# Optimization experiments

Hardware: AMD Instinct MI355X
Metric: run time of the kernel (lower is better)

## Reference

```python
import jax, jax.numpy as jnp
import numpy as np

N_NODES = 100000
N_EDGES = 300000
D = 256
N_LAYERS = 9
LN_EPS = 1e-5


def _mlp(h, w1, b1, w2, b2, ln_g, ln_b):
    # torch Linear: y = x @ W.T + b ; W is [out, in]
    h = jax.nn.relu(jnp.einsum('nd,hd->nh', h, w1) + b1)
    h = jnp.einsum('nh,oh->no', h, w2) + b2
    mu = jnp.mean(h, axis=-1, keepdims=True)
    var = jnp.mean(jnp.square(h - mu), axis=-1, keepdims=True)
    return (h - mu) * jax.lax.rsqrt(var + LN_EPS) * ln_g + ln_b


def setup_inputs() -> dict:
    key = jax.random.key(0)
    ks = jax.random.split(key, 16)
    s = 0.05  # small init scale for numerical sanity across 9 layers
    inp = {
        'x': jax.random.normal(ks[0], (N_NODES, D), dtype=jnp.float32),
        'edge_attr': jax.random.normal(ks[1], (N_EDGES, D), dtype=jnp.float32),
        'edge_fc1_w': jax.random.normal(ks[2], (N_LAYERS, D, D), dtype=jnp.float32) * s,
        'edge_fc1_b': jnp.zeros((N_LAYERS, D), dtype=jnp.float32),
        'edge_fc2_w': jax.random.normal(ks[3], (N_LAYERS, D, D), dtype=jnp.float32) * s,
        'edge_fc2_b': jnp.zeros((N_LAYERS, D), dtype=jnp.float32),
        'edge_ln_g': jnp.ones((N_LAYERS, D), dtype=jnp.float32),
        'edge_ln_b': jnp.zeros((N_LAYERS, D), dtype=jnp.float32),
        'node_fc1_w': jax.random.normal(ks[4], (N_LAYERS, D, D), dtype=jnp.float32) * s,
        'node_fc1_b': jnp.zeros((N_LAYERS, D), dtype=jnp.float32),
        'node_fc2_w': jax.random.normal(ks[5], (N_LAYERS, D, D), dtype=jnp.float32) * s,
        'node_fc2_b': jnp.zeros((N_LAYERS, D), dtype=jnp.float32),
        'node_ln_g': jnp.ones((N_LAYERS, D), dtype=jnp.float32),
        'node_ln_b': jnp.zeros((N_LAYERS, D), dtype=jnp.float32),
        'edge_index': jax.random.randint(ks[6], (2, N_EDGES), 0, N_NODES, dtype=jnp.int32),
    }
    return inp


def reference(x, edge_attr, edge_fc1_w, edge_fc1_b, edge_fc2_w, edge_fc2_b,
              edge_ln_g, edge_ln_b, node_fc1_w, node_fc1_b, node_fc2_w, node_fc2_b,
              node_ln_g, node_ln_b, edge_index):
    src = edge_index[0]  # x_j
    tgt = edge_index[1]  # aggregation target (aggr='add')
    for l in range(N_LAYERS):
        # edge MLP is applied to the ORIGINAL edge_attr in every layer
        e = _mlp(edge_attr, edge_fc1_w[l], edge_fc1_b[l], edge_fc2_w[l], edge_fc2_b[l],
                 edge_ln_g[l], edge_ln_b[l])
        msg = x[src] + e                               # [E, D] gather + add
        aggr = jax.ops.segment_sum(msg, tgt, num_segments=N_NODES)  # scatter-add
        upd = _mlp(aggr, node_fc1_w[l], node_fc1_b[l], node_fc2_w[l], node_fc2_b[l],
                   node_ln_g[l], node_ln_b[l])
        x = upd + x                                    # residual
    return x
```

## Files before the change

kernel.cpp:

```cpp
#include <hip/hip_runtime.h>
#include <stdint.h>

#define DD 256
#define NEDGE 300000
#define NNODE 100000
#define NLAY 9
#define LN_EPS 1e-5f

typedef __attribute__((ext_vector_type(8))) short bf16x8;
typedef __attribute__((ext_vector_type(4))) short s16x4;
typedef __attribute__((ext_vector_type(4))) float f32x4;
typedef __attribute__((ext_vector_type(4))) int i32x4;

static __device__ __forceinline__ short f2bf(float f) {
  union { float f; uint32_t u; } v; v.f = f;
  uint32_t r = (v.u + 0x7FFFu + ((v.u >> 16) & 1u)) >> 16;
  return (short)(uint16_t)r;
}
static __device__ __forceinline__ float bf2f(short s) {
  union { uint32_t u; float f; } v; v.u = ((uint32_t)(uint16_t)s) << 16;
  return v.f;
}
static __device__ __forceinline__ int addbf2(int a, int b) {
  const float a0 = bf2f((short)(a & 0xffff)), a1 = bf2f((short)(((uint32_t)a) >> 16));
  const float b0 = bf2f((short)(b & 0xffff)), b1 = bf2f((short)(((uint32_t)b) >> 16));
  const uint16_t r0 = (uint16_t)f2bf(a0 + b0), r1 = (uint16_t)f2bf(a1 + b1);
  return (int)(((uint32_t)r1 << 16) | r0);
}

static __device__ __forceinline__ void gld16(const void* g, void* l) {
  __builtin_amdgcn_global_load_lds((const __attribute__((address_space(1))) void*)g,
                                   (__attribute__((address_space(3))) void*)l, 16, 0, 0);
}

__global__ void cvtw_kernel(const float* __restrict__ src, short* __restrict__ dst, int nmat) {
  const int total = nmat * 8192;
  for (int j = blockIdx.x * blockDim.x + threadIdx.x; j < total; j += gridDim.x * blockDim.x) {
    const int m = j >> 13;
    const int jj = j & 8191;
    const int col = jj & 255;
    const int kq = jj >> 8;
    const float* s = src + (size_t)m * 65536 + col * 256 + kq * 8;
    const f32x4 u0 = *(const f32x4*)(s);
    const f32x4 u1 = *(const f32x4*)(s + 4);
    bf16x8 o;
#pragma unroll
    for (int q = 0; q < 4; ++q) { o[q] = f2bf(u0[q]); o[q + 4] = f2bf(u1[q]); }
    *(bf16x8*)(dst + (size_t)j * 8) = o;
  }
}

template<bool A_BF16, bool NODE>
__global__ __launch_bounds__(512, 4) void mlp_kernel(
    const void* __restrict__ Ain, const int* __restrict__ rowmap,
    const int* __restrict__ offs, const int* __restrict__ ssrc,
    const short* __restrict__ XbIn,
    const short* __restrict__ W1t, const short* __restrict__ W2t,
    const float* __restrict__ B1, const float* __restrict__ B2,
    const float* __restrict__ LG, const float* __restrict__ LB,
    short* __restrict__ OutB, float* __restrict__ OutF,
    short* __restrict__ XbOut, int M) {
  extern __shared__ char smem[];
  char* Abuf = smem + 32768;
  float* redbuf = (float*)(smem + 65536);
  const int tid = threadIdx.x;
  const int lane = tid & 63;
  const int wv = tid >> 6;
  const int wm = wv >> 2, wn = wv & 3;
  const int l15 = lane & 15, lq = lane >> 4;
  const int cbase = wn * 64;
  const int r0 = blockIdx.x * 64;

  auto stageW = [&](const short* Wt, int s, int slot) {
#pragma unroll
    for (int j = 0; j < 2; ++j) {
      const int c = tid + 512 * j;
      gld16(Wt + ((size_t)s * 1024 + c) * 8, smem + slot * 16384 + c * 16);
    }
  };

  stageW(W1t, 0, 0);

  if (NODE) {
    const short* efs = (const short*)Ain;
    const int r = tid & 63;
    const int j = tid >> 6;
    const int n = min(r0 + r, M - 1);
    const int beg = offs[n], end = offs[n + 1];
    float s[4][8];
#pragma unroll
    for (int c = 0; c < 4; ++c)
#pragma unroll
      for (int q = 0; q < 8; ++q) s[c][q] = 0.f;
    for (int p = beg; p < end; ++p) {
      const int src = ssrc[p];
#pragma unroll
      for (int c = 0; c < 4; ++c) {
        const int kq = j * 4 + c;
        const bf16x8 ev = *(const bf16x8*)(efs + (size_t)p * DD + kq * 8);
        const bf16x8 xv = *(const bf16x8*)(XbIn + (size_t)src * DD + kq * 8);
#pragma unroll
        for (int q = 0; q < 8; ++q) s[c][q] += bf2f(ev[q]) + bf2f(xv[q]);
      }
    }
#pragma unroll
    for (int c = 0; c < 4; ++c) {
      const int kq = j * 4 + c;
      bf16x8 o;
#pragma unroll
      for (int q = 0; q < 8; ++q) o[q] = f2bf(s[c][q]);
      *(bf16x8*)(Abuf + (kq * 64 + r) * 16) = o;
    }
  } else if (A_BF16) {
    const short* A = (const short*)Ain;
#pragma unroll
    for (int j = 0; j < 4; ++j) {
      const int c = tid + 512 * j;
      const int row = c & 63, kq = c >> 6;
      const int gr = min(r0 + row, M - 1);
      gld16(A + (size_t)gr * DD + kq * 8, Abuf + c * 16);
    }
  } else {
    const float* A = (const float*)Ain;
#pragma unroll
    for (int j = 0; j < 4; ++j) {
      const int c = tid + 512 * j;
      const int row = c & 63, kq = c >> 6;
      const int gr0 = min(r0 + row, M - 1);
      const int gr = rowmap ? rowmap[gr0] : gr0;
      const f32x4 u0 = *(const f32x4*)(A + (size_t)gr * DD + kq * 8);
      const f32x4 u1 = *(const f32x4*)(A + (size_t)gr * DD + kq * 8 + 4);
      bf16x8 o;
#pragma unroll
      for (int q = 0; q < 4; ++q) { o[q] = f2bf(u0[q]); o[q + 4] = f2bf(u1[q]); }
      *(bf16x8*)(Abuf + c * 16) = o;
    }
  }
  __syncthreads();

  f32x4 acc[2][4];
#pragma unroll
  for (int mi = 0; mi < 2; ++mi)
#pragma unroll
    for (int ni = 0; ni < 4; ++ni) acc[mi][ni] = (f32x4){0.f, 0.f, 0.f, 0.f};

#pragma unroll
  for (int s = 0; s < 8; ++s) {
    if (s < 7) stageW(W1t, s + 1, (s + 1) & 1);
    else       stageW(W2t, 0, 0);
    const char* wb = smem + (s & 1) * 16384;
    bf16x8 a[2], b[4];
#pragma unroll
    for (int mi = 0; mi < 2; ++mi)
      a[mi] = *(const bf16x8*)(Abuf + (((s * 4 + lq) * 64) + wm * 32 + mi * 16 + l15) * 16);
#pragma unroll
    for (int ni = 0; ni < 4; ++ni)
      b[ni] = *(const bf16x8*)(wb + lq * 4096 + (cbase + ni * 16 + l15) * 16);
#pragma unroll
    for (int ni = 0; ni < 4; ++ni)
#pragma unroll
      for (int mi = 0; mi < 2; ++mi)
        acc[mi][ni] = __builtin_amdgcn_mfma_f32_16x16x32_bf16(b[ni], a[mi], acc[mi][ni], 0, 0, 0);
    __syncthreads();
  }

  short* hid = (short*)Abuf;
  {
    f32x4 b1q[4];
#pragma unroll
    for (int ni = 0; ni < 4; ++ni)
      b1q[ni] = *(const f32x4*)(B1 + cbase + ni * 16 + lq * 4);
#pragma unroll
    for (int mi = 0; mi < 2; ++mi) {
      const int r = wm * 32 + mi * 16 + l15;
#pragma unroll
      for (int ni = 0; ni < 4; ++ni) {
        const int c4 = cbase + ni * 16 + lq * 4;
        s16x4 o;
#pragma unroll
        for (int i = 0; i < 4; ++i) {
          o[i] = f2bf(fmaxf(acc[mi][ni][i] + b1q[ni][i], 0.f));
          acc[mi][ni][i] = 0.f;
        }
        *(s16x4*)((char*)hid + r * 512 + (((c4 >> 3) ^ (r & 7)) << 4) + (c4 & 7) * 2) = o;
      }
    }
  }
  __syncthreads();

#pragma unroll
  for (int s = 0; s < 8; ++s) {
    if (s < 7) stageW(W2t, s + 1, (s + 1) & 1);
    const char* wb = smem + (s & 1) * 16384;
    bf16x8 a[2], b[4];
#pragma unroll
    for (int mi = 0; mi < 2; ++mi) {
      const int r = wm * 32 + mi * 16 + l15;
      a[mi] = *(const bf16x8*)((const char*)hid + r * 512 + ((((s * 4 + lq)) ^ (r & 7)) << 4));
    }
#pragma unroll
    for (int ni = 0; ni < 4; ++ni)
      b[ni] = *(const bf16x8*)(wb + lq * 4096 + (cbase + ni * 16 + l15) * 16);
#pragma unroll
    for (int ni = 0; ni < 4; ++ni)
#pragma unroll
      for (int mi = 0; mi < 2; ++mi)
        acc[mi][ni] = __builtin_amdgcn_mfma_f32_16x16x32_bf16(b[ni], a[mi], acc[mi][ni], 0, 0, 0);
    __syncthreads();
  }

  f32x4 b2q[4];
#pragma unroll
  for (int ni = 0; ni < 4; ++ni)
    b2q[ni] = *(const f32x4*)(B2 + cbase + ni * 16 + lq * 4);
  float mean_[2], inv_[2];
#pragma unroll
  for (int mi = 0; mi < 2; ++mi) {
    float s1 = 0.f, s2 = 0.f;
#pragma unroll
    for (int ni = 0; ni < 4; ++ni)
#pragma unroll
      for (int i = 0; i < 4; ++i) {
        const float v = acc[mi][ni][i] + b2q[ni][i];
        s1 += v; s2 += v * v;
      }
    s1 += __shfl_xor(s1, 16); s2 += __shfl_xor(s2, 16);
    s1 += __shfl_xor(s1, 32); s2 += __shfl_xor(s2, 32);
    mean_[mi] = s1; inv_[mi] = s2;
  }
  if (lq == 0) {
#pragma unroll
    for (int mi = 0; mi < 2; ++mi) {
      const int r = wm * 32 + mi * 16 + l15;
      redbuf[(r * 4 + wn) * 2 + 0] = mean_[mi];
      redbuf[(r * 4 + wn) * 2 + 1] = inv_[mi];
    }
  }
  __syncthreads();
#pragma unroll
  for (int mi = 0; mi < 2; ++mi) {
    const int r = wm * 32 + mi * 16 + l15;
    float t1 = 0.f, t2 = 0.f;
#pragma unroll
    for (int w = 0; w < 4; ++w) {
      t1 += redbuf[(r * 4 + w) * 2 + 0];
      t2 += redbuf[(r * 4 + w) * 2 + 1];
    }
    const float mean = t1 * (1.f / 256.f);
    const float var = t2 * (1.f / 256.f) - mean * mean;
    mean_[mi] = mean;
    inv_[mi] = rsqrtf(var + LN_EPS);
  }

  f32x4 gq[4], bq[4];
#pragma unroll
  for (int ni = 0; ni < 4; ++ni) {
    gq[ni] = *(const f32x4*)(LG + cbase + ni * 16 + lq * 4);
    bq[ni] = *(const f32x4*)(LB + cbase + ni * 16 + lq * 4);
  }

  if (NODE) {
    const bool wantF = (OutF != nullptr);
    if (!wantF) {
      short* ob = (short*)Abuf;
#pragma unroll
      for (int mi = 0; mi < 2; ++mi) {
        const int r = wm * 32 + mi * 16 + l15;
#pragma unroll
        for (int ni = 0; ni < 4; ++ni) {
          const int c4 = cbase + ni * 16 + lq * 4;
          s16x4 o;
#pragma unroll
          for (int i = 0; i < 4; ++i)
            o[i] = f2bf((acc[mi][ni][i] + b2q[ni][i] - mean_[mi]) * inv_[mi] * gq[ni][i] + bq[ni][i]);
          *(s16x4*)((char*)ob + r * 512 + (((c4 >> 3) ^ (r & 7)) << 4) + (c4 & 7) * 2) = o;
        }
      }
      __syncthreads();
#pragma unroll
      for (int j = 0; j < 4; ++j) {
        const int gg = tid + 512 * j;
        const int row = gg >> 5, Lg = gg & 31;
        const int grow = r0 + row;
        if (grow < M) {
          const i32x4 yv = *(const i32x4*)((const short*)ob + row * DD + ((Lg ^ (row & 7)) << 3));
          i32x4 xv = *(const i32x4*)(XbIn + (size_t)grow * DD + Lg * 8);
#pragma unroll
          for (int q = 0; q < 4; ++q) xv[q] = addbf2(yv[q], xv[q]);
          *(i32x4*)(XbOut + (size_t)grow * DD + Lg * 8) = xv;
        }
      }
    } else {
      float* ob = (float*)Abuf;
#pragma unroll
      for (int h = 0; h < 2; ++h) {
        if ((cbase >> 7) == h) {
#pragma unroll
          for (int mi = 0; mi < 2; ++mi) {
            const int r = wm * 32 + mi * 16 + l15;
#pragma unroll
            for (int ni = 0; ni < 4; ++ni) {
              const int cl4 = cbase - h * 128 + ni * 16 + lq * 4;
              f32x4 y;
#pragma unroll
              for (int i = 0; i < 4; ++i)
                y[i] = (acc[mi][ni][i] + b2q[ni][i] - mean_[mi]) * inv_[mi] * gq[ni][i] + bq[ni][i];
              *(f32x4*)((char*)ob + r * 512 + ((((cl4 >> 2) ^ (r & 7))) << 4)) = y;
            }
          }
        }
        __syncthreads();
#pragma unroll
        for (int j = 0; j < 4; ++j) {
          const int gg = tid + 512 * j;
          const int row = gg >> 5, Lc = gg & 31;
          const int grow = r0 + row;
          if (grow < M) {
            f32x4 v = *(const f32x4*)(ob + row * 128 + ((Lc ^ (row & 7)) << 2));
            const s16x4 xr = *(const s16x4*)(XbIn + (size_t)grow * DD + h * 128 + Lc * 4);
            v.x += bf2f(xr.x); v.y += bf2f(xr.y); v.z += bf2f(xr.z); v.w += bf2f(xr.w);
            *(f32x4*)(OutF + (size_t)grow * DD + h * 128 + Lc * 4) = v;
          }
        }
        if (h == 0) __syncthreads();
      }
    }
  } else {
    short* ob = (short*)Abuf;
#pragma unroll
    for (int mi = 0; mi < 2; ++mi) {
      const int r = wm * 32 + mi * 16 + l15;
#pragma unroll
      for (int ni = 0; ni < 4; ++ni) {
        const int c4 = cbase + ni * 16 + lq * 4;
        s16x4 o;
#pragma unroll
        for (int i = 0; i < 4; ++i)
          o[i] = f2bf((acc[mi][ni][i] + b2q[ni][i] - mean_[mi]) * inv_[mi] * gq[ni][i] + bq[ni][i]);
        *(s16x4*)((char*)ob + r * 512 + (((c4 >> 3) ^ (r & 7)) << 4) + (c4 & 7) * 2) = o;
      }
    }
    __syncthreads();
#pragma unroll
    for (int j = 0; j < 4; ++j) {
      const int gg = tid + 512 * j;
      const int row = gg >> 5, Lg = gg & 31;
      const int grow = r0 + row;
      if (grow < M) {
        const i32x4 v = *(const i32x4*)((const short*)ob + row * DD + ((Lg ^ (row & 7)) << 3));
        *(i32x4*)(OutB + (size_t)grow * DD + Lg * 8) = v;
      }
    }
  }
}

__global__ void count_kernel(const int* __restrict__ tgt, int* __restrict__ deg) {
  const int e = blockIdx.x * 256 + threadIdx.x;
  if (e < NEDGE) atomicAdd(&deg[tgt[e]], 1);
}

__global__ __launch_bounds__(256) void scan1_kernel(
    const int* __restrict__ deg, int* __restrict__ locex, int* __restrict__ bsum) {
  __shared__ int sh[256];
  const int t = threadIdx.x, b = blockIdx.x;
  const int idx = b * 256 + t;
  const int v = (idx < NNODE) ? deg[idx] : 0;
  sh[t] = v;
  __syncthreads();
#pragma unroll
  for (int off = 1; off < 256; off <<= 1) {
    const int add = (t >= off) ? sh[t - off] : 0;
    __syncthreads();
    sh[t] += add;
    __syncthreads();
  }
  if (idx < NNODE) locex[idx] = sh[t] - v;
  if (t == 255) bsum[b] = sh[255];
}

__global__ __launch_bounds__(512) void scan2_kernel(int* __restrict__ bsum, int nb) {
  __shared__ int sh[512];
  const int t = threadIdx.x;
  const int v = (t < nb) ? bsum[t] : 0;
  sh[t] = v;
  __syncthreads();
#pragma unroll
  for (int off = 1; off < 512; off <<= 1) {
    const int add = (t >= off) ? sh[t - off] : 0;
    __syncthreads();
    sh[t] += add;
    __syncthreads();
  }
  if (t < nb) bsum[t] = sh[t] - v;
}

__global__ __launch_bounds__(256) void scan3_kernel(
    const int* __restrict__ locex, const int* __restrict__ bsum,
    int* __restrict__ offs, int* __restrict__ cur) {
  const int idx = blockIdx.x * 256 + threadIdx.x;
  if (idx < NNODE) {
    const int o = locex[idx] + bsum[blockIdx.x];
    offs[idx] = o;
    cur[idx] = o;
  }
  if (idx == 0) offs[NNODE] = NEDGE;
}

__global__ void fill_kernel(const int* __restrict__ src, const int* __restrict__ tgt,
                            int* cur, int* seid, int* ssrc) {
  const int e = blockIdx.x * 256 + threadIdx.x;
  if (e < NEDGE) {
    const int t = tgt[e];
    const int p = atomicAdd(&cur[t], 1);
    seid[p] = e;
    ssrc[p] = src[e];
  }
}

__global__ void cvt4_kernel(const float* __restrict__ src, short* __restrict__ dst, int n4) {
  for (int i = blockIdx.x * blockDim.x + threadIdx.x; i < n4; i += gridDim.x * blockDim.x) {
    const f32x4 v = ((const f32x4*)src)[i];
    s16x4 o;
    o.x = f2bf(v.x); o.y = f2bf(v.y); o.z = f2bf(v.z); o.w = f2bf(v.w);
    ((s16x4*)dst)[i] = o;
  }
}

__global__ __launch_bounds__(256) void gather_cvt_kernel(
    const float* __restrict__ src, const int* __restrict__ perm,
    short* __restrict__ dst, int n) {
  const int w = (blockIdx.x * blockDim.x + threadIdx.x) >> 6;
  if (w >= n) return;
  const int lane = threadIdx.x & 63;
  const f32x4 v = *(const f32x4*)(src + (size_t)perm[w] * DD + lane * 4);
  s16x4 o; o.x = f2bf(v.x); o.y = f2bf(v.y); o.z = f2bf(v.z); o.w = f2bf(v.w);
  *(s16x4*)(dst + (size_t)w * DD + lane * 4) = o;
}

extern "C" void kernel_launch(void* const* d_in, const int* in_sizes, int n_in,
                              void* d_out, int out_size, void* d_ws, size_t ws_size,
                              hipStream_t stream) {
  const float* x_in = (const float*)d_in[0];
  const float* ea_f = (const float*)d_in[1];
  const float* e1w = (const float*)d_in[2];
  const float* e1b = (const float*)d_in[3];
  const float* e2w = (const float*)d_in[4];
  const float* e2b = (const float*)d_in[5];
  const float* elg = (const float*)d_in[6];
  const float* elb = (const float*)d_in[7];
  const float* n1w = (const float*)d_in[8];
  const float* n1b = (const float*)d_in[9];
  const float* n2w = (const float*)d_in[10];
  const float* n2b = (const float*)d_in[11];
  const float* nlg = (const float*)d_in[12];
  const float* nlb = (const float*)d_in[13];
  const int* eidx = (const int*)d_in[14];
  float* x = (float*)d_out;

  char* p = (char*)d_ws;
  auto take = [&](size_t bytes) {
    char* r = p;
    p += (bytes + 255) & ~(size_t)255;
    return r;
  };
  short* efeat = (short*)take((size_t)NEDGE * DD * 2);
  short* xbA = (short*)take((size_t)NNODE * DD * 2);
  short* xbB = (short*)take((size_t)NNODE * DD * 2);
  short* we1t = (short*)take((size_t)NLAY * DD * DD * 2);
  short* we2t = (short*)take((size_t)NLAY * DD * DD * 2);
  short* wn1t = (short*)take((size_t)NLAY * DD * DD * 2);
  short* wn2t = (short*)take((size_t)NLAY * DD * DD * 2);
  int* deg = (int*)take((size_t)NNODE * 4);
  int* offs = (int*)take((size_t)(NNODE + 1) * 4);
  int* cur = (int*)take((size_t)NNODE * 4);
  int* seid = (int*)take((size_t)NEDGE * 4);
  int* ssrc = (int*)take((size_t)NEDGE * 4);
  int* locex = (int*)take((size_t)(NNODE + 256) * 4);
  int* bsum = (int*)take(512 * 4);
  short* eab = (short*)take((size_t)NEDGE * DD * 2);
  const bool use_eab = ((size_t)(p - (char*)d_ws) <= ws_size);

  const int SMEM = 67584;
  hipFuncSetAttribute((const void*)mlp_kernel<true, false>,
                      hipFuncAttributeMaxDynamicSharedMemorySize, SMEM);
  hipFuncSetAttribute((const void*)mlp_kernel<false, false>,
                      hipFuncAttributeMaxDynamicSharedMemorySize, SMEM);
  hipFuncSetAttribute((const void*)mlp_kernel<true, true>,
                      hipFuncAttributeMaxDynamicSharedMemorySize, SMEM);

  cvtw_kernel<<<288, 256, 0, stream>>>(e1w, we1t, NLAY);
  cvtw_kernel<<<288, 256, 0, stream>>>(e2w, we2t, NLAY);
  cvtw_kernel<<<288, 256, 0, stream>>>(n1w, wn1t, NLAY);
  cvtw_kernel<<<288, 256, 0, stream>>>(n2w, wn2t, NLAY);
  cvt4_kernel<<<2048, 256, 0, stream>>>(x_in, xbA, NNODE * DD / 4);

  const int NB = (NNODE + 255) / 256;
  hipMemsetAsync(deg, 0, (size_t)NNODE * 4, stream);
  count_kernel<<<(NEDGE + 255) / 256, 256, 0, stream>>>(eidx + NEDGE, deg);
  scan1_kernel<<<NB, 256, 0, stream>>>(deg, locex, bsum);
  scan2_kernel<<<1, 512, 0, stream>>>(bsum, NB);
  scan3_kernel<<<NB, 256, 0, stream>>>(locex, bsum, offs, cur);
  fill_kernel<<<(NEDGE + 255) / 256, 256, 0, stream>>>(eidx, eidx + NEDGE, cur, seid, ssrc);
  if (use_eab)
    gather_cvt_kernel<<<NEDGE / 4, 256, 0, stream>>>(ea_f, seid, eab, NEDGE);

  const int egrid = (NEDGE + 63) / 64;
  const int ngrid = (NNODE + 63) / 64;
  short* xin = xbA;
  short* xout = xbB;
  for (int l = 0; l < NLAY; ++l) {
    if (use_eab) {
      mlp_kernel<true, false><<<egrid, 512, SMEM, stream>>>(
          eab, nullptr, nullptr, nullptr, nullptr,
          we1t + l * 65536, we2t + l * 65536, e1b + l * DD,
          e2b + l * DD, elg + l * DD, elb + l * DD, efeat, nullptr,
          nullptr, NEDGE);
    } else {
      mlp_kernel<false, false><<<egrid, 512, SMEM, stream>>>(
          ea_f, seid, nullptr, nullptr, nullptr,
          we1t + l * 65536, we2t + l * 65536, e1b + l * DD,
          e2b + l * DD, elg + l * DD, elb + l * DD, efeat, nullptr,
          nullptr, NEDGE);
    }
    mlp_kernel<true, true><<<ngrid, 512, SMEM, stream>>>(
        efeat, nullptr, offs, ssrc, xin,
        wn1t + l * 65536, wn2t + l * 65536, n1b + l * DD,
        n2b + l * DD, nlg + l * DD, nlb + l * DD, nullptr,
        (l == NLAY - 1) ? x : nullptr, xout, NNODE);
    short* t = xin; xin = xout; xout = t;
  }
  (void)in_sizes; (void)n_in; (void)out_size; (void)ws_size;
}
```

Before: 2.579 ms.

## Add dedicated 1024-thread edge MLP kernel with 16 waves per 64-row tile

Adds a specialized edge MLP kernel that runs 1024 threads (16 waves, 2x8 wave grid) per 64-row tile instead of the generic 512-thread mlp_kernel. Each wave computes a 32x32 output block, so per-wave work halves and the block double-buffers weight slices with global_load_lds. The aim is more parallelism and latency hiding on the edge MLP, which dominates runtime. The cost is more barrier synchronization per block, more shared memory, and lower per-wave reuse of the A and B fragments.

Result: slower. 3.072 ms (+19.1%).

```diff
diff --git a/kernel.cpp b/kernel.cpp
--- a/kernel.cpp
+++ b/kernel.cpp
@@ -47,6 +47,206 @@
 #pragma unroll
     for (int q = 0; q < 4; ++q) { o[q] = f2bf(u0[q]); o[q + 4] = f2bf(u1[q]); }
     *(bf16x8*)(dst + (size_t)j * 8) = o;
+  }
+}
+
+template<bool A_BF16>
+__global__ __launch_bounds__(1024, 8) void edge_kernel(
+    const void* __restrict__ Ain, const int* __restrict__ rowmap,
+    const short* __restrict__ W1t, const short* __restrict__ W2t,
+    const float* __restrict__ B1, const float* __restrict__ B2,
+    const float* __restrict__ LG, const float* __restrict__ LB,
+    short* __restrict__ OutB, int M) {
+  extern __shared__ char smem[];
+  char* Abuf = smem + 32768;
+  float* redbuf = (float*)(smem + 65536);
+  const int tid = threadIdx.x;
+  const int lane = tid & 63;
+  const int wv = tid >> 6;
+  const int wm = wv >> 3, wn = wv & 7;
+  const int l15 = lane & 15, lq = lane >> 4;
+  const int cbase = wn * 32;
+  const int r0 = blockIdx.x * 64;
+
+  auto stageW = [&](const short* Wt, int s, int slot) {
+    gld16(Wt + ((size_t)s * 1024 + tid) * 8, smem + slot * 16384 + tid * 16);
+  };
+
+  stageW(W1t, 0, 0);
+
+  if (A_BF16) {
+    const short* A = (const short*)Ain;
+#pragma unroll
+    for (int j = 0; j < 2; ++j) {
+      const int c = tid + 1024 * j;
+      const int row = c & 63, kq = c >> 6;
+      const int gr = min(r0 + row, M - 1);
+      gld16(A + (size_t)gr * DD + kq * 8, Abuf + c * 16);
+    }
+  } else {
+    const float* A = (const float*)Ain;
+#pragma unroll
+    for (int j = 0; j < 2; ++j) {
+      const int c = tid + 1024 * j;
+      const int row = c & 63, kq = c >> 6;
+      const int gr0 = min(r0 + row, M - 1);
+      const int gr = rowmap ? rowmap[gr0] : gr0;
+      const f32x4 u0 = *(const f32x4*)(A + (size_t)gr * DD + kq * 8);
+      const f32x4 u1 = *(const f32x4*)(A + (size_t)gr * DD + kq * 8 + 4);
+      bf16x8 o;
+#pragma unroll
+      for (int q = 0; q < 4; ++q) { o[q] = f2bf(u0[q]); o[q + 4] = f2bf(u1[q]); }
+      *(bf16x8*)(Abuf + c * 16) = o;
+    }
+  }
+  __syncthreads();
+
+  f32x4 acc[2][2];
+#pragma unroll
+  for (int mi = 0; mi < 2; ++mi)
+#pragma unroll
+    for (int ni = 0; ni < 2; ++ni) acc[mi][ni] = (f32x4){0.f, 0.f, 0.f, 0.f};
+
+#pragma unroll
+  for (int s = 0; s < 8; ++s) {
+    if (s < 7) stageW(W1t, s + 1, (s + 1) & 1);
+    else       stageW(W2t, 0, 0);
+    const char* wb = smem + (s & 1) * 16384;
+    bf16x8 a[2], b[2];
+#pragma unroll
+    for (int mi = 0; mi < 2; ++mi) {
+      const int row = wm * 32 + mi * 16 + l15;
+      a[mi] = *(const bf16x8*)(Abuf + (((s * 4 + lq) * 64) + row) * 16);
+    }
+#pragma unroll
+    for (int ni = 0; ni < 2; ++ni)
+      b[ni] = *(const bf16x8*)(wb + lq * 4096 + (cbase + ni * 16 + l15) * 16);
+#pragma unroll
+    for (int ni = 0; ni < 2; ++ni)
+#pragma unroll
+      for (int mi = 0; mi < 2; ++mi)
+        acc[mi][ni] = __builtin_amdgcn_mfma_f32_16x16x32_bf16(b[ni], a[mi], acc[mi][ni], 0, 0, 0);
+    __syncthreads();
+  }
+
+  short* hid = (short*)Abuf;
+  {
+    f32x4 b1q[2];
+#pragma unroll
+    for (int ni = 0; ni < 2; ++ni)
+      b1q[ni] = *(const f32x4*)(B1 + cbase + ni * 16 + lq * 4);
+#pragma unroll
+    for (int mi = 0; mi < 2; ++mi) {
+      const int r = wm * 32 + mi * 16 + l15;
+#pragma unroll
+      for (int ni = 0; ni < 2; ++ni) {
+        const int c4 = cbase + ni * 16 + lq * 4;
+        s16x4 o;
+#pragma unroll
+        for (int i = 0; i < 4; ++i) {
+          o[i] = f2bf(fmaxf(acc[mi][ni][i] + b1q[ni][i], 0.f));
+          acc[mi][ni][i] = 0.f;
+        }
+        *(s16x4*)((char*)hid + r * 512 + (((c4 >> 3) ^ (r & 7)) << 4) + (c4 & 7) * 2) = o;
+      }
+    }
+  }
+  __syncthreads();
+
+#pragma unroll
+  for (int s = 0; s < 8; ++s) {
+    if (s < 7) stageW(W2t, s + 1, (s + 1) & 1);
+    const char* wb = smem + (s & 1) * 16384;
+    bf16x8 a[2], b[2];
+#pragma unroll
+    for (int mi = 0; mi < 2; ++mi) {
+      const int r = wm * 32 + mi * 16 + l15;
+      a[mi] = *(const bf16x8*)((const char*)hid + r * 512 + ((((s * 4 + lq)) ^ (r & 7)) << 4));
+    }
+#pragma unroll
+    for (int ni = 0; ni < 2; ++ni)
+      b[ni] = *(const bf16x8*)(wb + lq * 4096 + (cbase + ni * 16 + l15) * 16);
+#pragma unroll
+    for (int ni = 0; ni < 2; ++ni)
+#pragma unroll
+      for (int mi = 0; mi < 2; ++mi)
+        acc[mi][ni] = __builtin_amdgcn_mfma_f32_16x16x32_bf16(b[ni], a[mi], acc[mi][ni], 0, 0, 0);
+    __syncthreads();
+  }
+
+  f32x4 b2q[2];
+#pragma unroll
+  for (int ni = 0; ni < 2; ++ni)
+    b2q[ni] = *(const f32x4*)(B2 + cbase + ni * 16 + lq * 4);
+  float mean_[2], inv_[2];
+#pragma unroll
+  for (int mi = 0; mi < 2; ++mi) {
+    float s1 = 0.f, s2 = 0.f;
+#pragma unroll
+    for (int ni = 0; ni < 2; ++ni)
+#pragma unroll
+      for (int i = 0; i < 4; ++i) {
+        const float v = acc[mi][ni][i] + b2q[ni][i];
+        s1 += v; s2 += v * v;
+      }
+    s1 += __shfl_xor(s1, 16); s2 += __shfl_xor(s2, 16);
+    s1 += __shfl_xor(s1, 32); s2 += __shfl_xor(s2, 32);
+    mean_[mi] = s1; inv_[mi] = s2;
+  }
+  if (lq == 0) {
+#pragma unroll
+    for (int mi = 0; mi < 2; ++mi) {
+      const int r = wm * 32 + mi * 16 + l15;
+      redbuf[(r * 8 + wn) * 2 + 0] = mean_[mi];
+      redbuf[(r * 8 + wn) * 2 + 1] = inv_[mi];
+    }
+  }
+  __syncthreads();
+#pragma unroll
+  for (int mi = 0; mi < 2; ++mi) {
+    const int r = wm * 32 + mi * 16 + l15;
+    float t1 = 0.f, t2 = 0.f;
+#pragma unroll
+    for (int w = 0; w < 8; ++w) {
+      t1 += redbuf[(r * 8 + w) * 2 + 0];
+      t2 += redbuf[(r * 8 + w) * 2 + 1];
+    }
+    const float mean = t1 * (1.f / 256.f);
+    const float var = t2 * (1.f / 256.f) - mean * mean;
+    mean_[mi] = mean;
+    inv_[mi] = rsqrtf(var + LN_EPS);
+  }
+
+  f32x4 gq[2], bq[2];
+#pragma unroll
+  for (int ni = 0; ni < 2; ++ni) {
+    gq[ni] = *(const f32x4*)(LG + cbase + ni * 16 + lq * 4);
+    bq[ni] = *(const f32x4*)(LB + cbase + ni * 16 + lq * 4);
+  }
+  short* ob = (short*)Abuf;
+#pragma unroll
+  for (int mi = 0; mi < 2; ++mi) {
+    const int r = wm * 32 + mi * 16 + l15;
+#pragma unroll
+    for (int ni = 0; ni < 2; ++ni) {
+      const int c4 = cbase + ni * 16 + lq * 4;
+      s16x4 o;
+#pragma unroll
+      for (int i = 0; i < 4; ++i)
+        o[i] = f2bf((acc[mi][ni][i] + b2q[ni][i] - mean_[mi]) * inv_[mi] * gq[ni][i] + bq[ni][i]);
+      *(s16x4*)((char*)ob + r * 512 + (((c4 >> 3) ^ (r & 7)) << 4) + (c4 & 7) * 2) = o;
+    }
+  }
+  __syncthreads();
+#pragma unroll
+  for (int j = 0; j < 2; ++j) {
+    const int gg = tid + 1024 * j;
+    const int row = gg >> 5, Lg = gg & 31;
+    const int grow = r0 + row;
+    if (grow < M) {
+      const i32x4 v = *(const i32x4*)((const short*)ob + row * DD + ((Lg ^ (row & 7)) << 3));
+      *(i32x4*)(OutB + (size_t)grow * DD + Lg * 8) = v;
+    }
   }
 }
 
@@ -480,13 +680,14 @@
   short* eab = (short*)take((size_t)NEDGE * DD * 2);
   const bool use_eab = ((size_t)(p - (char*)d_ws) <= ws_size);
 
-  const int SMEM = 67584;
-  hipFuncSetAttribute((const void*)mlp_kernel<true, false>,
-                      hipFuncAttributeMaxDynamicSharedMemorySize, SMEM);
-  hipFuncSetAttribute((const void*)mlp_kernel<false, false>,
-                      hipFuncAttributeMaxDynamicSharedMemorySize, SMEM);
+  const int SMEM_E = 69632;
+  const int SMEM_N = 67584;
+  hipFuncSetAttribute((const void*)edge_kernel<true>,
+                      hipFuncAttributeMaxDynamicSharedMemorySize, SMEM_E);
+  hipFuncSetAttribute((const void*)edge_kernel<false>,
+                      hipFuncAttributeMaxDynamicSharedMemorySize, SMEM_E);
   hipFuncSetAttribute((const void*)mlp_kernel<true, true>,
-                      hipFuncAttributeMaxDynamicSharedMemorySize, SMEM);
+                      hipFuncAttributeMaxDynamicSharedMemorySize, SMEM_N);
 
   cvtw_kernel<<<288, 256, 0, stream>>>(e1w, we1t, NLAY);
   cvtw_kernel<<<288, 256, 0, stream>>>(e2w, we2t, NLAY);
@@ -510,19 +711,15 @@
   short* xout = xbB;
   for (int l = 0; l < NLAY; ++l) {
     if (use_eab) {
-      mlp_kernel<true, false><<<egrid, 512, SMEM, stream>>>(
-          eab, nullptr, nullptr, nullptr, nullptr,
-          we1t + l * 65536, we2t + l * 65536, e1b + l * DD,
-          e2b + l * DD, elg + l * DD, elb + l * DD, efeat, nullptr,
-          nullptr, NEDGE);
+      edge_kernel<true><<<egrid, 1024, SMEM_E, stream>>>(
+          eab, nullptr, we1t + l * 65536, we2t + l * 65536, e1b + l * DD,
+          e2b + l * DD, elg + l * DD, elb + l * DD, efeat, NEDGE);
     } else {
-      mlp_kernel<false, false><<<egrid, 512, SMEM, stream>>>(
-          ea_f, seid, nullptr, nullptr, nullptr,
-          we1t + l * 65536, we2t + l * 65536, e1b + l * DD,
-          e2b + l * DD, elg + l * DD, elb + l * DD, efeat, nullptr,
-          nullptr, NEDGE);
-    }
-    mlp_kernel<true, true><<<ngrid, 512, SMEM, stream>>>(
+      edge_kernel<false><<<egrid, 1024, SMEM_E, stream>>>(
+          ea_f, seid, we1t + l * 65536, we2t + l * 65536, e1b + l * DD,
+          e2b + l * DD, elg + l * DD, elb + l * DD, efeat, NEDGE);
+    }
+    mlp_kernel<true, true><<<ngrid, 512, SMEM_N, stream>>>(
         efeat, nullptr, offs, ssrc, xin,
         wn1t + l * 65536, wn2t + l * 65536, n1b + l * DD,
         n2b + l * DD, nlg + l * DD, nlb + l * DD, nullptr,
```
